# Optimization experiments

Hardware: AMD Instinct MI355X
Metric: run time of the kernel (lower is better)

## Reference

```python
import jax, jax.numpy as jnp
import numpy as np

B, S, H, E, I, MAX_K, A_HID = 2, 2048, 1024, 8, 2688, 6, 50


def setup_inputs() -> dict:
    key = jax.random.key(0)
    ks = jax.random.split(key, 10)
    sc = 0.02
    return {
        "hidden_states": jax.random.normal(ks[0], (B, S, H), dtype=jnp.float32),
        "router_w": jax.random.normal(ks[1], (E, H), dtype=jnp.float32) * sc,
        "actor_w1": jax.random.normal(ks[2], (A_HID, H), dtype=jnp.float32) * sc,
        "actor_b1": jnp.zeros((A_HID,), dtype=jnp.float32),
        "actor_w2": jax.random.normal(ks[3], (MAX_K, A_HID), dtype=jnp.float32) * sc,
        "actor_b2": jnp.zeros((MAX_K,), dtype=jnp.float32),
        "gate_w": jax.random.normal(ks[4], (E, I, H), dtype=jnp.float32) * sc,
        "up_w": jax.random.normal(ks[5], (E, I, H), dtype=jnp.float32) * sc,
        "down_w": jax.random.normal(ks[6], (E, H, I), dtype=jnp.float32) * sc,
    }


def reference(hidden_states, router_w, actor_w1, actor_b1, actor_w2, actor_b2,
              gate_w, up_w, down_w):
    # Router: frozen linear -> softmax probs  [B,S,E]
    probs = jax.nn.softmax(
        jnp.einsum("bsh,eh->bse", hidden_states, router_w).astype(jnp.float32),
        axis=-1)

    # Allocator (ActorCritic.actor): Linear -> GELU -> Linear, clamp(-30,30)
    a_h = jax.nn.gelu(jnp.einsum("bsh,ah->bsa", hidden_states, actor_w1) + actor_b1)
    actor_logits = jnp.clip(
        jnp.einsum("bsa,ka->bsk", a_h, actor_w2) + actor_b2, -30.0, 30.0)
    # deterministic per-token k in [1, MAX_K]
    sampled_k = jnp.argmax(actor_logits, axis=-1) + 1  # [B,S] int

    # dynamic_topk_indices_and_scores: iterative argmax+scatter == select the
    # k highest-prob experts per token; keep their scores, zero elsewhere.
    order = jnp.argsort(-probs, axis=-1)           # descending order of experts
    rank = jnp.argsort(order, axis=-1)             # rank[e] = position of expert e
    mask = rank < sampled_k[..., None]             # [B,S,E] bool, top-k selected
    scores = jnp.where(mask, probs, 0.0).astype(hidden_states.dtype)

    # Expert dispatch-combine: out = sum_e scores[...,e] * LlamaMLP_e(x)
    out = jnp.zeros_like(hidden_states)
    for e in range(E):  # fixed small loop over experts
        g = jnp.einsum("bsh,ih->bsi", hidden_states, gate_w[e])
        u = jnp.einsum("bsh,ih->bsi", hidden_states, up_w[e])
        y = jnp.einsum("bsi,hi->bsh", jax.nn.silu(g) * u, down_w[e])
        out = out + scores[..., e:e + 1] * y
    return out
```

## Files before the change

### kernel.cpp

```cpp
#include <hip/hip_runtime.h>
#include <hip/hip_bf16.h>
#include <stdint.h>

#define TOK 4096
#define HD  1024
#define NE  8
#define ID  2688
#define MAXK 6
#define AHID 50
#define NROW 58
#define KCH 64
#define NCH (HD / KCH)

#define BM 128
#define BN 128
#define BK 64
#define NTM (TOK / BM)
#define NID2 (2 * ID)
#define NTN_GUC (NID2 / BN)
#define NB_GUC (NTN_GUC * NTM)
#define NTN_D (HD / BN)
#define NB_D (NTN_D * NTM)
#define CVTB 384

typedef float  f32x4  __attribute__((ext_vector_type(4)));
typedef __bf16 bf16x8 __attribute__((ext_vector_type(8)));
typedef ushort ushort8v __attribute__((ext_vector_type(8)));

__device__ __forceinline__ ushort f2bf(float f) {
  union { float f; uint32_t u; } v; v.f = f;
  return (ushort)((v.u + 0x7FFFu + ((v.u >> 16) & 1u)) >> 16);
}
__device__ __forceinline__ float bf2f(ushort u) {
  union { uint32_t u; float f; } v; v.u = (uint32_t)u << 16; return v.f;
}

#define GLD_LDS16(gp, lp)                                                      \
  __builtin_amdgcn_global_load_lds(                                            \
      (const __attribute__((address_space(1))) uint32_t*)(uintptr_t)(gp),      \
      (__attribute__((address_space(3))) uint32_t*)(uint32_t)(uintptr_t)(lp),  \
      16, 0, 0)

__global__ void k_cvt(const float* __restrict__ src, ushort* __restrict__ dst, int n) {
  int idx = blockIdx.x * blockDim.x + threadIdx.x;
  int stride = gridDim.x * blockDim.x;
  for (int i = idx * 8; i < n; i += stride * 8) {
    float4 a = *(const float4*)(src + i);
    float4 b = *(const float4*)(src + i + 4);
    ushort8v o;
    o[0] = f2bf(a.x); o[1] = f2bf(a.y); o[2] = f2bf(a.z); o[3] = f2bf(a.w);
    o[4] = f2bf(b.x); o[5] = f2bf(b.y); o[6] = f2bf(b.z); o[7] = f2bf(b.w);
    *(ushort8v*)(dst + i) = o;
  }
}

__global__ void k_cvt_gu(const float* __restrict__ g, const float* __restrict__ u,
                         ushort* __restrict__ dst) {
  const int total = NE * NID2 * (HD / 8);
  int idx = blockIdx.x * blockDim.x + threadIdx.x;
  int stride = gridDim.x * blockDim.x;
  for (int i8 = idx; i8 < total; i8 += stride) {
    const int col = (i8 & (HD / 8 - 1)) * 8;
    const int row = i8 >> 7;
    const int e = row / NID2;
    const int q = row - e * NID2;
    const int p = q >> 7, r = q & 127;
    const float* src = ((r < 64) ? g + ((size_t)e * ID + p * 64 + r) * HD
                                 : u + ((size_t)e * ID + p * 64 + (r - 64)) * HD) + col;
    float4 a = *(const float4*)(src);
    float4 b = *(const float4*)(src + 4);
    ushort8v o;
    o[0] = f2bf(a.x); o[1] = f2bf(a.y); o[2] = f2bf(a.z); o[3] = f2bf(a.w);
    o[4] = f2bf(b.x); o[5] = f2bf(b.y); o[6] = f2bf(b.z); o[7] = f2bf(b.w);
    *(ushort8v*)(dst + (size_t)row * HD + col) = o;
  }
}

__global__ __launch_bounds__(256) void k_logits(
    const float* __restrict__ x, const float* __restrict__ rw,
    const float* __restrict__ aw1, float* __restrict__ partial,
    ushort* __restrict__ Xb) {
  __shared__ float xs[256][KCH + 1];
  const int tid = threadIdx.x;
  const int t0 = blockIdx.x * 256;
  const int c = blockIdx.y;
  const int k0 = c * KCH;
#pragma unroll
  for (int j = 0; j < 16; ++j) {
    const int id4 = j * 256 + tid;
    const int row = id4 >> 4;
    const int c4 = (id4 & 15) * 4;
    float4 v = *(const float4*)(x + (size_t)(t0 + row) * HD + k0 + c4);
    xs[row][c4 + 0] = v.x; xs[row][c4 + 1] = v.y;
    xs[row][c4 + 2] = v.z; xs[row][c4 + 3] = v.w;
    ushort4 o; o.x = f2bf(v.x); o.y = f2bf(v.y); o.z = f2bf(v.z); o.w = f2bf(v.w);
    *(ushort4*)(Xb + (size_t)(t0 + row) * HD + k0 + c4) = o;
  }
  __syncthreads();
  float acc[NROW];
#pragma unroll
  for (int r = 0; r < NROW; ++r) acc[r] = 0.f;
  for (int k4 = 0; k4 < KCH; k4 += 4) {
    const float x0 = xs[tid][k4 + 0], x1 = xs[tid][k4 + 1];
    const float x2 = xs[tid][k4 + 2], x3 = xs[tid][k4 + 3];
#pragma unroll
    for (int r = 0; r < NROW; ++r) {
      const float* wp = ((r < NE) ? (rw + (size_t)r * HD)
                                  : (aw1 + (size_t)(r - NE) * HD)) + k0 + k4;
      acc[r] += x0 * wp[0] + x1 * wp[1] + x2 * wp[2] + x3 * wp[3];
    }
  }
  const int t = t0 + tid;
#pragma unroll
  for (int r = 0; r < NROW; ++r)
    partial[((size_t)c * NROW + r) * TOK + t] = acc[r];
}

__global__ __launch_bounds__(256) void k_reduce(
    const float* __restrict__ partial, float* __restrict__ dots) {
  const int t = blockIdx.x * 256 + threadIdx.x;
  const int r = blockIdx.y;
  float s = 0.f;
#pragma unroll
  for (int c = 0; c < NCH; ++c)
    s += partial[((size_t)c * NROW + r) * TOK + t];
  dots[(size_t)r * TOK + t] = s;
}

__global__ __launch_bounds__(64) void k_select(
    const float* __restrict__ dots, const float* __restrict__ ab1_,
    const float* __restrict__ aw2_, const float* __restrict__ ab2_,
    float* __restrict__ scores, int* __restrict__ idx, int* __restrict__ cnt) {
  const int lane = threadIdx.x;
  const int t = blockIdx.x * 64 + lane;
  float d[NROW];
#pragma unroll
  for (int r = 0; r < NROW; ++r) d[r] = dots[(size_t)r * TOK + t];
  float m = d[0];
#pragma unroll
  for (int e = 1; e < NE; ++e) m = fmaxf(m, d[e]);
  float p[NE]; float sum = 0.f;
#pragma unroll
  for (int e = 0; e < NE; ++e) { p[e] = expf(d[e] - m); sum += p[e]; }
  float inv = 1.f / sum;
#pragma unroll
  for (int e = 0; e < NE; ++e) p[e] *= inv;
  float lg[MAXK];
#pragma unroll
  for (int k = 0; k < MAXK; ++k) lg[k] = ab2_[k];
#pragma unroll
  for (int i = 0; i < AHID; ++i) {
    float v = d[NE + i] + ab1_[i];
    float g = 0.5f * v * (1.f + tanhf(0.7978845608028654f * (v + 0.044715f * v * v * v)));
#pragma unroll
    for (int k = 0; k < MAXK; ++k) lg[k] += g * aw2_[k * AHID + i];
  }
  int best = 0; float bv = fminf(fmaxf(lg[0], -30.f), 30.f);
#pragma unroll
  for (int k = 1; k < MAXK; ++k) {
    float lv = fminf(fmaxf(lg[k], -30.f), 30.f);
    if (lv > bv) { bv = lv; best = k; }
  }
  const int kk = best + 1;
  float sc[NE];
#pragma unroll
  for (int e = 0; e < NE; ++e) {
    int rank = 0;
#pragma unroll
    for (int j = 0; j < NE; ++j)
      rank += (p[j] > p[e]) || (p[j] == p[e] && j < e);
    sc[e] = (rank < kk) ? p[e] : 0.f;
    scores[(size_t)t * NE + e] = sc[e];
  }
#pragma unroll
  for (int e = 0; e < NE; ++e) {
    unsigned long long msk = __ballot(sc[e] > 0.f);
    int npop = __popcll(msk);
    int mypos = __popcll(msk & ((1ull << lane) - 1ull));
    int base = 0;
    if (lane == 0 && npop) base = atomicAdd(cnt + e, npop);
    base = __shfl(base, 0);
    if (sc[e] > 0.f) idx[e * TOK + base + mypos] = t;
  }
}

__global__ __launch_bounds__(256, 2) void k_gateupC(
    const ushort* __restrict__ X, const int* __restrict__ idx,
    const int* __restrict__ cnt, const ushort* __restrict__ Wc,
    ushort* __restrict__ act, const int e0, const int actStrideRows,
    const float* __restrict__ dwsrc, ushort* __restrict__ dwdst) {
  __shared__ __attribute__((aligned(16))) ushort lds[BM * BK + BN * BK];
  ushort* As = lds;
  ushort* Bs = lds + BM * BK;

  const int bid = blockIdx.x;
  if (bid >= NB_GUC) {
    if (blockIdx.z != 0) return;
    const int cb = bid - NB_GUC;
    const int ncvt = NE * HD * ID;
    const int stride = CVTB * 256 * 8;
    for (int i = (cb * 256 + threadIdx.x) * 8; i < ncvt; i += stride) {
      float4 a = *(const float4*)(dwsrc + i);
      float4 b = *(const float4*)(dwsrc + i + 4);
      ushort8v o;
      o[0] = f2bf(a.x); o[1] = f2bf(a.y); o[2] = f2bf(a.z); o[3] = f2bf(a.w);
      o[4] = f2bf(b.x); o[5] = f2bf(b.y); o[6] = f2bf(b.z); o[7] = f2bf(b.w);
      *(ushort8v*)(dwdst + i) = o;
    }
    return;
  }

  const int e = e0 + blockIdx.z;
  const int n = cnt[e];
  const int logical = (bid & 7) * (NB_GUC / 8) + (bid >> 3);
  const int tn = logical >> 5;
  const int tm = logical & (NTM - 1);
  const int row0 = tm * BM;
  if (row0 >= n) return;
  const int* idx_e = idx + e * TOK;
  const ushort* WcE = Wc + (size_t)e * NID2 * HD;
  ushort* actE = act + (size_t)actStrideRows * e * ID;

  const int tid = threadIdx.x;
  const int lane = tid & 63;
  const int w = tid >> 6;
  const int wr = (w >> 1) * 64;
  const int wc = (w & 1) * 64;
  const int srow = lane >> 3;
  const int scol = ((lane & 7) ^ srow) * 8;
  const int col0 = tn * BN;

  f32x4 acc[4][4] = {};

  const ushort* pa[4]; const ushort* pb[4];
  ushort* la[4]; ushort* lb[4];
#pragma unroll
  for (int j = 0; j < 4; ++j) {
    const int cc = w * 4 + j;
    const int r = cc * 8 + srow;
    const int token = idx_e[min(row0 + r, n - 1)];
    pa[j] = X   + (size_t)token * HD + scol;
    pb[j] = WcE + (size_t)(col0 + r) * HD + scol;
    la[j] = &As[cc * 512]; lb[j] = &Bs[cc * 512];
  }

  for (int kt = 0; kt < HD / BK; ++kt) {
    const int k0 = kt * BK;
    __syncthreads();
#pragma unroll
    for (int j = 0; j < 4; ++j) {
      GLD_LDS16(pa[j] + k0, la[j]);
      GLD_LDS16(pb[j] + k0, lb[j]);
    }
    __syncthreads();
#pragma unroll
    for (int kk = 0; kk < 2; ++kk) {
      const int kc = kk * 32 + (lane >> 4) * 8;
      const int rr = lane & 15;
      const int kcs = (((kc >> 3) ^ (rr & 7)) << 3);
      bf16x8 af[4], bf_[4];
#pragma unroll
      for (int m = 0; m < 4; ++m)
        af[m] = *(const bf16x8*)&As[(wr + m * 16 + rr) * BK + kcs];
#pragma unroll
      for (int nn = 0; nn < 4; ++nn)
        bf_[nn] = *(const bf16x8*)&Bs[(wc + nn * 16 + rr) * BK + kcs];
#pragma unroll
      for (int m = 0; m < 4; ++m)
#pragma unroll
        for (int nn = 0; nn < 4; ++nn)
          acc[m][nn] = __builtin_amdgcn_mfma_f32_16x16x32_bf16(af[m], bf_[nn], acc[m][nn], 0, 0, 0);
    }
  }

  const int erow = (lane >> 4) * 4, ecol = lane & 15;
  float* exch = (float*)lds;
  __syncthreads();
  if (w & 1) {
#pragma unroll
    for (int m = 0; m < 4; ++m) {
      const int rbase = wr + m * 16 + erow;
#pragma unroll
      for (int nn = 0; nn < 4; ++nn) {
        const int c = nn * 16 + ecol;
#pragma unroll
        for (int j = 0; j < 4; ++j)
          exch[(rbase + j) * 64 + c] = acc[m][nn][j];
      }
    }
  }
  __syncthreads();
  if (!(w & 1)) {
#pragma unroll
    for (int m = 0; m < 4; ++m) {
      const int rbase = wr + m * 16 + erow;
#pragma unroll
      for (int nn = 0; nn < 4; ++nn) {
        const int c = nn * 16 + ecol;
        const int gc = tn * 64 + c;
#pragma unroll
        for (int j = 0; j < 4; ++j) {
          float g = acc[m][nn][j];
          float u = exch[(rbase + j) * 64 + c];
          float h = (g / (1.f + __expf(-g))) * u;
          actE[(size_t)(row0 + rbase + j) * ID + gc] = f2bf(h);
        }
      }
    }
  }
}

__global__ __launch_bounds__(256, 2) void k_down(
    const ushort* __restrict__ act, const ushort* __restrict__ Wd,
    const int* __restrict__ idx, const int* __restrict__ cnt,
    ushort* __restrict__ y) {
  __shared__ __attribute__((aligned(16))) ushort As[BM * BK];
  __shared__ __attribute__((aligned(16))) ushort Bs[BN * BK];

  const int e = blockIdx.z;
  const int n = cnt[e];
  const int bid = blockIdx.x;
  const int logical = (bid & 7) * (NB_D / 8) + (bid >> 3);
  const int tn = logical >> 5;
  const int tm = logical & (NTM - 1);
  const int row0 = tm * BM;
  if (row0 >= n) return;
  const int* idx_e = idx + e * TOK;
  const ushort* A = act + (size_t)e * TOK * ID;
  const ushort* W = Wd + (size_t)e * HD * ID;
  ushort* yE = y + (size_t)e * TOK * HD;

  const int tid = threadIdx.x;
  const int lane = tid & 63;
  const int w = tid >> 6;
  const int wr = (w >> 1) * 64;
  const int wc = (w & 1) * 64;
  const int srow = lane >> 3;
  const int scol = ((lane & 7) ^ srow) * 8;
  const int col0 = tn * BN;

  f32x4 acc[4][4] = {};

  const ushort* pa[4]; const ushort* pb[4];
  ushort* la[4]; ushort* lb[4];
#pragma unroll
  for (int j = 0; j < 4; ++j) {
    const int cc = w * 4 + j;
    const int r = cc * 8 + srow;
    pa[j] = A + (size_t)min(row0 + r, n - 1) * ID + scol;
    pb[j] = W + (size_t)(col0 + r) * ID + scol;
    la[j] = &As[cc * 512]; lb[j] = &Bs[cc * 512];
  }

  for (int kt = 0; kt < ID / BK; ++kt) {
    const int k0 = kt * BK;
    __syncthreads();
#pragma unroll
    for (int j = 0; j < 4; ++j) {
      GLD_LDS16(pa[j] + k0, la[j]);
      GLD_LDS16(pb[j] + k0, lb[j]);
    }
    __syncthreads();
#pragma unroll
    for (int kk = 0; kk < 2; ++kk) {
      const int kc = kk * 32 + (lane >> 4) * 8;
      const int rr = lane & 15;
      const int kcs = (((kc >> 3) ^ (rr & 7)) << 3);
      bf16x8 af[4], bf_[4];
#pragma unroll
      for (int m = 0; m < 4; ++m)
        af[m] = *(const bf16x8*)&As[(wr + m * 16 + rr) * BK + kcs];
#pragma unroll
      for (int nn = 0; nn < 4; ++nn)
        bf_[nn] = *(const bf16x8*)&Bs[(wc + nn * 16 + rr) * BK + kcs];
#pragma unroll
      for (int m = 0; m < 4; ++m)
#pragma unroll
        for (int nn = 0; nn < 4; ++nn)
          acc[m][nn] = __builtin_amdgcn_mfma_f32_16x16x32_bf16(af[m], bf_[nn], acc[m][nn], 0, 0, 0);
    }
  }

  const int erow = (lane >> 4) * 4, ecol = lane & 15;
#pragma unroll
  for (int m = 0; m < 4; ++m) {
    const int cr0 = row0 + wr + m * 16 + erow;
#pragma unroll
    for (int j = 0; j < 4; ++j) {
      const int cr = cr0 + j;
      if (cr < n) {
        const int token = idx_e[cr];
        ushort* yp = yE + (size_t)token * HD + col0 + wc;
#pragma unroll
        for (int nn = 0; nn < 4; ++nn)
          yp[nn * 16 + ecol] = f2bf(acc[m][nn][j]);
      }
    }
  }
}

__global__ __launch_bounds__(256) void k_combine(
    const ushort* __restrict__ y, const float* __restrict__ scores,
    float* __restrict__ out) {
  const int w = threadIdx.x >> 6, lane = threadIdx.x & 63;
  const int t = blockIdx.x * 4 + w;
  const int c0 = lane * 16;
  float acc[16];
#pragma unroll
  for (int i = 0; i < 16; ++i) acc[i] = 0.f;
  const float* sc = scores + (size_t)t * NE;
#pragma unroll
  for (int e = 0; e < NE; ++e) {
    const float s = sc[e];
    if (s > 0.f) {
      const ushort8v* yp = (const ushort8v*)(y + ((size_t)e * TOK + t) * HD + c0);
      ushort8v v0 = yp[0], v1 = yp[1];
#pragma unroll
      for (int i = 0; i < 8; ++i) acc[i] += s * bf2f(v0[i]);
#pragma unroll
      for (int i = 0; i < 8; ++i) acc[8 + i] += s * bf2f(v1[i]);
    }
  }
  float* op = out + (size_t)t * HD + c0;
#pragma unroll
  for (int i = 0; i < 4; ++i)
    *(float4*)(op + 4 * i) = make_float4(acc[4*i], acc[4*i+1], acc[4*i+2], acc[4*i+3]);
}

__global__ __launch_bounds__(256) void k_down64(
    const ushort* __restrict__ act, const ushort* __restrict__ Wd,
    const float* __restrict__ scores, const int* __restrict__ idx,
    const int* __restrict__ cnt, const int e, float* __restrict__ out) {
  __shared__ __attribute__((aligned(16))) ushort As[64 * 64];
  __shared__ __attribute__((aligned(16))) ushort Bs[64 * 64];
  const int n = cnt[e];
  const int row0 = blockIdx.y * 64;
  if (row0 >= n) return;
  const int* idx_e = idx + e * TOK;
  const ushort* A = act;
  const ushort* W = Wd + (size_t)e * HD * ID;
  const int col0 = blockIdx.x * 64;
  const int tid = threadIdx.x, lane = tid & 63, w = tid >> 6;
  const int wr = (w >> 1) * 32, wc = (w & 1) * 32;
  const int srow = lane >> 3, scol = (lane & 7) * 8;
  f32x4 acc[2][2] = {};
  const ushort* pa[2]; const ushort* pb[2];
  ushort* la[2]; ushort* lb[2];
#pragma unroll
  for (int j = 0; j < 2; ++j) {
    const int cc = w * 2 + j;
    const int r = cc * 8 + srow;
    pa[j] = A + (size_t)min(row0 + r, n - 1) * ID + scol;
    pb[j] = W + (size_t)(col0 + r) * ID + scol;
    la[j] = &As[cc * 512]; lb[j] = &Bs[cc * 512];
  }
  for (int kt = 0; kt < ID / 64; ++kt) {
    const int k0 = kt * 64;
    __syncthreads();
#pragma unroll
    for (int j = 0; j < 2; ++j) { GLD_LDS16(pa[j] + k0, la[j]); GLD_LDS16(pb[j] + k0, lb[j]); }
    __syncthreads();
#pragma unroll
    for (int kk = 0; kk < 2; ++kk) {
      const int kc = kk * 32 + (lane >> 4) * 8;
      const int rr = lane & 15;
      bf16x8 af[2], bf_[2];
#pragma unroll
      for (int m = 0; m < 2; ++m) af[m] = *(const bf16x8*)&As[(wr + m * 16 + rr) * 64 + kc];
#pragma unroll
      for (int nn = 0; nn < 2; ++nn) bf_[nn] = *(const bf16x8*)&Bs[(wc + nn * 16 + rr) * 64 + kc];
#pragma unroll
      for (int m = 0; m < 2; ++m)
#pragma unroll
        for (int nn = 0; nn < 2; ++nn)
          acc[m][nn] = __builtin_amdgcn_mfma_f32_16x16x32_bf16(af[m], bf_[nn], acc[m][nn], 0, 0, 0);
    }
  }
  const int erow = (lane >> 4) * 4, ecol = lane & 15;
#pragma unroll
  for (int m = 0; m < 2; ++m) {
    const int cr0 = row0 + wr + m * 16 + erow;
#pragma unroll
    for (int j = 0; j < 4; ++j) {
      const int cr = cr0 + j;
      if (cr < n) {
        const int token = idx_e[cr];
        const float s = scores[(size_t)token * NE + e];
        float* op = out + (size_t)token * HD + col0 + wc;
#pragma unroll
        for (int nn = 0; nn < 2; ++nn) op[nn * 16 + ecol] += s * acc[m][nn][j];
      }
    }
  }
}

extern "C" void kernel_launch(void* const* d_in, const int* in_sizes, int n_in,
                              void* d_out, int out_size, void* d_ws, size_t ws_size,
                              hipStream_t stream) {
  const float* hs       = (const float*)d_in[0];
  const float* router_w = (const float*)d_in[1];
  const float* actor_w1 = (const float*)d_in[2];
  const float* actor_b1 = (const float*)d_in[3];
  const float* actor_w2 = (const float*)d_in[4];
  const float* actor_b2 = (const float*)d_in[5];
  const float* gate_w   = (const float*)d_in[6];
  const float* up_w     = (const float*)d_in[7];
  const float* down_w   = (const float*)d_in[8];
  float* out = (float*)d_out;

  const size_t sz_x    = (size_t)TOK * HD * 2;
  const size_t sz_w    = (size_t)NE * ID * HD * 2;
  const size_t sz_wgu  = 2 * sz_w;
  const size_t sz_act1 = (size_t)TOK * ID * 2;
  const size_t sz_actC = (size_t)NE * TOK * ID * 2;
  const size_t sz_part = (size_t)NCH * NROW * TOK * 4;
  const size_t sz_dt   = (size_t)NROW * TOK * 4;
  const size_t sz_sc   = (size_t)TOK * NE * 4;
  const size_t sz_ix   = (size_t)NE * TOK * 4;

  const size_t fixed = sz_x + sz_wgu + sz_w;
  const size_t tail  = sz_dt + sz_sc + sz_ix + 256;
  const size_t fb_act = (sz_act1 > sz_part ? sz_act1 : sz_part);
  const size_t need_fb = fixed + fb_act + tail;
  const size_t need_cb = fixed + sz_actC + tail;
  if (ws_size < need_fb) return;
  const bool combined = (ws_size >= need_cb);
  const size_t act_sz = combined ? sz_actC : fb_act;

  char* ws = (char*)d_ws;
  ushort* Xb  = (ushort*)ws;
  ushort* Wgu = (ushort*)(ws + sz_x);
  ushort* Wdb = (ushort*)(ws + sz_x + sz_wgu);
  ushort* yb  = Wgu;
  ushort* act = (ushort*)(ws + fixed);
  float*  partial = (float*)(ws + fixed);
  float*  dots   = (float*)(ws + fixed + act_sz);
  float*  scores = (float*)(ws + fixed + act_sz + sz_dt);
  int*    idx    = (int*)  (ws + fixed + act_sz + sz_dt + sz_sc);
  int*    cnt    = (int*)  (ws + fixed + act_sz + sz_dt + sz_sc + sz_ix);

  hipMemsetAsync(cnt, 0, NE * 4, stream);

  k_cvt_gu<<<2048, 256, 0, stream>>>(gate_w, up_w, Wgu);

  k_logits<<<dim3(TOK / 256, NCH), 256, 0, stream>>>(hs, router_w, actor_w1, partial, Xb);
  k_reduce<<<dim3(TOK / 256, NROW), 256, 0, stream>>>(partial, dots);
  k_select<<<TOK / 64, 64, 0, stream>>>(dots, actor_b1, actor_w2, actor_b2,
                                        scores, idx, cnt);

  if (combined) {
    k_gateupC<<<dim3(NB_GUC + CVTB, 1, NE), 256, 0, stream>>>(
        Xb, idx, cnt, Wgu, act, 0, TOK, down_w, Wdb);
    k_down<<<dim3(NB_D, 1, NE), 256, 0, stream>>>(act, Wdb, idx, cnt, yb);
    k_combine<<<TOK / 4, 256, 0, stream>>>(yb, scores, out);
  } else {
    hipMemsetAsync(out, 0, (size_t)TOK * HD * 4, stream);
    k_cvt<<<2048, 256, 0, stream>>>(down_w, Wdb, NE * ID * HD);
    for (int e = 0; e < NE; ++e) {
      k_gateupC<<<dim3(NB_GUC, 1, 1), 256, 0, stream>>>(
          Xb, idx, cnt, Wgu, act, e, 0, nullptr, nullptr);
      k_down64<<<dim3(HD / 64, TOK / 64), 256, 0, stream>>>(
          act, Wdb, scores, idx, cnt, e, out);
    }
  }
}
```

Before: 480.9 us.

## Replace expert GEMMs with 256x256-tile, 8-wave, double-buffered pipelined kernels

The gate/up and down expert GEMMs move from 128x128 tiles with 4 waves and a load-sync-compute loop to 256x256 tiles with 8 waves. They use a double-buffered LDS stage split into k-halves, so async global-to-LDS loads for the next step overlap MFMA work, with explicit vmcnt waits, barriers and s_setprio around the MFMA bursts. The larger tile raises data reuse per block and cuts the number of blocks. The tradeoff is 128KB of LDS per block, fewer blocks for small expert token counts, and a more complex hand-scheduled pipeline that could raise register pressure.

```diff
diff --git a/kernel.cpp b/kernel.cpp
--- a/kernel.cpp
+++ b/kernel.cpp
@@ -19,9 +19,10 @@
 #define NID2 (2 * ID)
 #define NTN_GUC (NID2 / BN)
 #define NB_GUC (NTN_GUC * NTM)
-#define NTN_D (HD / BN)
-#define NB_D (NTN_D * NTM)
-#define CVTB 384
+#define CVTB8 160
+
+#define NB8_GU (21 * 16)
+#define NB8_D  (4 * 16)
 
 typedef float  f32x4  __attribute__((ext_vector_type(4)));
 typedef __bf16 bf16x8 __attribute__((ext_vector_type(8)));
@@ -184,22 +185,47 @@
   }
 }
 
-__global__ __launch_bounds__(256, 2) void k_gateupC(
+
+#define STG8(PTR0, PTR1, LBASE, koff)                                          \
+  do {                                                                         \
+    GLD_LDS16((PTR0) + (koff), (LBASE));                                       \
+    GLD_LDS16((PTR1) + (koff), (LBASE) + 512);                                 \
+  } while (0)
+
+#define PH8(kh_, q_, RDB_)                                                     \
+  {                                                                            \
+    const int reg_ = (buf * 2 + (kh_)) * 8192;                                 \
+    bf16x8 af_[4];                                                             \
+    _Pragma("unroll") for (int mm = 0; mm < 4; ++mm)                           \
+        af_[mm] = *(const bf16x8*)&SH[reg_ + baseA + ((q_)*64 + mm*16) * 32];  \
+    if (RDB_) {                                                                \
+      _Pragma("unroll") for (int nn = 0; nn < 4; ++nn)                         \
+          bfr[nn] = *(const bf16x8*)&SH[32768 + reg_ + baseB + nn * 16 * 32];  \
+    }                                                                          \
+    __builtin_amdgcn_s_barrier();                                              \
+    __builtin_amdgcn_s_setprio(1);                                             \
+    _Pragma("unroll") for (int mm = 0; mm < 4; ++mm)                           \
+    _Pragma("unroll") for (int nn = 0; nn < 4; ++nn)                           \
+        acc[(q_)*4 + mm][nn] = __builtin_amdgcn_mfma_f32_16x16x32_bf16(        \
+            af_[mm], bfr[nn], acc[(q_)*4 + mm][nn], 0, 0, 0);                  \
+    __builtin_amdgcn_s_setprio(0);                                             \
+    __builtin_amdgcn_s_barrier();                                              \
+  }
+
+__global__ __launch_bounds__(512, 2) void k_gateup8(
     const ushort* __restrict__ X, const int* __restrict__ idx,
     const int* __restrict__ cnt, const ushort* __restrict__ Wc,
-    ushort* __restrict__ act, const int e0, const int actStrideRows,
+    ushort* __restrict__ act,
     const float* __restrict__ dwsrc, ushort* __restrict__ dwdst) {
-  __shared__ __attribute__((aligned(16))) ushort lds[BM * BK + BN * BK];
-  ushort* As = lds;
-  ushort* Bs = lds + BM * BK;
+  __shared__ __attribute__((aligned(16))) ushort SH[65536];
 
   const int bid = blockIdx.x;
-  if (bid >= NB_GUC) {
+  if (bid >= NB8_GU) {
     if (blockIdx.z != 0) return;
-    const int cb = bid - NB_GUC;
+    const int cb = bid - NB8_GU;
     const int ncvt = NE * HD * ID;
-    const int stride = CVTB * 256 * 8;
-    for (int i = (cb * 256 + threadIdx.x) * 8; i < ncvt; i += stride) {
+    const int stride = CVTB8 * 512 * 8;
+    for (int i = (cb * 512 + (int)threadIdx.x) * 8; i < ncvt; i += stride) {
       float4 a = *(const float4*)(dwsrc + i);
       float4 b = *(const float4*)(dwsrc + i + 4);
       ushort8v o;
@@ -210,8 +236,235 @@
     return;
   }
 
-  const int e = e0 + blockIdx.z;
+  const int e = blockIdx.z;
   const int n = cnt[e];
+  const int logical = (bid & 7) * (NB8_GU / 8) + (bid >> 3);
+  const int tn = logical >> 4;
+  const int tm = logical & 15;
+  const int row0 = tm * 256;
+  if (row0 >= n) return;
+  const int* idx_e = idx + e * TOK;
+  const ushort* WcE = Wc + (size_t)e * NID2 * HD;
+  ushort* actE = act + (size_t)e * TOK * ID;
+  const int col0 = tn * 256;
+
+  const int tid = threadIdx.x;
+  const int lane = tid & 63;
+  const int w = tid >> 6;
+  const int wm = w >> 2;
+  const int wn = w & 3;
+
+  const int lr = lane >> 2;
+  const int swzS = (((lane & 3) ^ (lr & 3)) << 3);
+  const int rA0 = w * 32 + lr, rA1 = w * 32 + 16 + lr;
+  const ushort* pA0 = X + (size_t)idx_e[min(row0 + rA0, n - 1)] * HD + swzS;
+  const ushort* pA1 = X + (size_t)idx_e[min(row0 + rA1, n - 1)] * HD + swzS;
+  const ushort* pB0 = WcE + (size_t)(col0 + rA0) * HD + swzS;
+  const ushort* pB1 = WcE + (size_t)(col0 + rA1) * HD + swzS;
+  const int lgrp = (w * 32) * 32;
+
+  const int rl = lane & 15, gk = lane >> 4;
+  const int rsw = ((gk ^ (rl & 3)) << 3);
+  const int baseA = (wm * 128 + rl) * 32 + rsw;
+  const int baseB = (wn * 64 + rl) * 32 + rsw;
+
+  f32x4 acc[8][4] = {};
+  bf16x8 bfr[4];
+
+  const int NT = HD / BK;
+#define SA8(t_, kh_) STG8(pA0, pA1, SH + ((((t_)&1)*2 + (kh_)) * 8192) + lgrp, (t_)*BK + (kh_)*32)
+#define SB8(t_, kh_) STG8(pB0, pB1, SH + 32768 + ((((t_)&1)*2 + (kh_)) * 8192) + lgrp, (t_)*BK + (kh_)*32)
+
+  SA8(0, 0); SB8(0, 0); SA8(0, 1); SB8(0, 1);
+  SA8(1, 0); SB8(1, 0);
+  asm volatile("s_waitcnt vmcnt(4)" ::: "memory");
+  __builtin_amdgcn_s_barrier();
+
+  for (int t = 0; t < NT; ++t) {
+    const int buf = t & 1;
+    if (t + 1 < NT) SA8(t + 1, 1);
+    PH8(0, 0, 1)
+    if (t + 1 < NT) SB8(t + 1, 1);
+    PH8(0, 1, 0)
+    if (t + 2 < NT) SA8(t + 2, 0);
+    PH8(1, 0, 1)
+    if (t + 2 < NT) SB8(t + 2, 0);
+    if (t + 1 < NT) {
+      if (t + 2 < NT) { asm volatile("s_waitcnt vmcnt(4)" ::: "memory"); }
+      else            { asm volatile("s_waitcnt vmcnt(0)" ::: "memory"); }
+    }
+    PH8(1, 1, 0)
+  }
+#undef SA8
+#undef SB8
+
+  const int erow = (lane >> 4) * 4, ecol = lane & 15;
+  const int slot = wm * 2 + (wn >> 1);
+  float* exch = (float*)SH;
+  if (wn & 1) {
+#pragma unroll
+    for (int mm = 0; mm < 8; ++mm) {
+      const int rb = mm * 16 + erow;
+#pragma unroll
+      for (int nn = 0; nn < 4; ++nn) {
+        const int cc = nn * 16 + ecol;
+#pragma unroll
+        for (int j = 0; j < 4; ++j)
+          exch[(slot * 128 + rb + j) * 64 + cc] = acc[mm][nn][j];
+      }
+    }
+  }
+  __builtin_amdgcn_s_barrier();
+  if (!(wn & 1)) {
+    const int p = tn * 2 + (wn >> 1);
+#pragma unroll
+    for (int mm = 0; mm < 8; ++mm) {
+      const int rb = mm * 16 + erow;
+#pragma unroll
+      for (int nn = 0; nn < 4; ++nn) {
+        const int cc = nn * 16 + ecol;
+        const int gc = p * 64 + cc;
+#pragma unroll
+        for (int j = 0; j < 4; ++j) {
+          const int cr = row0 + wm * 128 + rb + j;
+          if (cr < n) {
+            float g = acc[mm][nn][j];
+            float u = exch[(slot * 128 + rb + j) * 64 + cc];
+            float h = (g / (1.f + __expf(-g))) * u;
+            actE[(size_t)cr * ID + gc] = f2bf(h);
+          }
+        }
+      }
+    }
+  }
+}
+
+__global__ __launch_bounds__(512, 2) void k_down8(
+    const ushort* __restrict__ act, const ushort* __restrict__ Wd,
+    const int* __restrict__ idx, const int* __restrict__ cnt,
+    ushort* __restrict__ y) {
+  __shared__ __attribute__((aligned(16))) ushort SH[65536];
+
+  const int e = blockIdx.z;
+  const int n = cnt[e];
+  const int bid = blockIdx.x;
+  const int logical = (bid & 7) * (NB8_D / 8) + (bid >> 3);
+  const int tn = logical >> 4;
+  const int tm = logical & 15;
+  const int row0 = tm * 256;
+  if (row0 >= n) return;
+  const int* idx_e = idx + e * TOK;
+  const ushort* A = act + (size_t)e * TOK * ID;
+  const ushort* W = Wd + (size_t)e * HD * ID;
+  ushort* yE = y + (size_t)e * TOK * HD;
+  const int col0 = tn * 256;
+
+  const int tid = threadIdx.x;
+  const int lane = tid & 63;
+  const int w = tid >> 6;
+  const int wm = w >> 2;
+  const int wn = w & 3;
+
+  const int lr = lane >> 2;
+  const int swzS = (((lane & 3) ^ (lr & 3)) << 3);
+  const int rA0 = w * 32 + lr, rA1 = w * 32 + 16 + lr;
+  const ushort* pA0 = A + (size_t)min(row0 + rA0, n - 1) * ID + swzS;
+  const ushort* pA1 = A + (size_t)min(row0 + rA1, n - 1) * ID + swzS;
+  const ushort* pB0 = W + (size_t)(col0 + rA0) * ID + swzS;
+  const ushort* pB1 = W + (size_t)(col0 + rA1) * ID + swzS;
+  const int lgrp = (w * 32) * 32;
+
+  const int rl = lane & 15, gk = lane >> 4;
+  const int rsw = ((gk ^ (rl & 3)) << 3);
+  const int baseA = (wm * 128 + rl) * 32 + rsw;
+  const int baseB = (wn * 64 + rl) * 32 + rsw;
+
+  f32x4 acc[8][4] = {};
+  bf16x8 bfr[4];
+
+  const int NT = ID / BK;
+#define SA8(t_, kh_) STG8(pA0, pA1, SH + ((((t_)&1)*2 + (kh_)) * 8192) + lgrp, (t_)*BK + (kh_)*32)
+#define SB8(t_, kh_) STG8(pB0, pB1, SH + 32768 + ((((t_)&1)*2 + (kh_)) * 8192) + lgrp, (t_)*BK + (kh_)*32)
+
+  SA8(0, 0); SB8(0, 0); SA8(0, 1); SB8(0, 1);
+  SA8(1, 0); SB8(1, 0);
+  asm volatile("s_waitcnt vmcnt(4)" ::: "memory");
+  __builtin_amdgcn_s_barrier();
+
+  for (int t = 0; t < NT; ++t) {
+    const int buf = t & 1;
+    if (t + 1 < NT) SA8(t + 1, 1);
+    PH8(0, 0, 1)
+    if (t + 1 < NT) SB8(t + 1, 1);
+    PH8(0, 1, 0)
+    if (t + 2 < NT) SA8(t + 2, 0);
+    PH8(1, 0, 1)
+    if (t + 2 < NT) SB8(t + 2, 0);
+    if (t + 1 < NT) {
+      if (t + 2 < NT) { asm volatile("s_waitcnt vmcnt(4)" ::: "memory"); }
+      else            { asm volatile("s_waitcnt vmcnt(0)" ::: "memory"); }
+    }
+    PH8(1, 1, 0)
+  }
+#undef SA8
+#undef SB8
+
+  const int erow = (lane >> 4) * 4, ecol = lane & 15;
+#pragma unroll
+  for (int mm = 0; mm < 8; ++mm) {
+    const int cr0 = row0 + wm * 128 + mm * 16 + erow;
+#pragma unroll
+    for (int j = 0; j < 4; ++j) {
+      const int cr = cr0 + j;
+      if (cr < n) {
+        const int token = idx_e[cr];
+        ushort* yp = yE + (size_t)token * HD + col0 + wn * 64;
+#pragma unroll
+        for (int nn = 0; nn < 4; ++nn)
+          yp[nn * 16 + ecol] = f2bf(acc[mm][nn][j]);
+      }
+    }
+  }
+}
+
+__global__ __launch_bounds__(256) void k_combine(
+    const ushort* __restrict__ y, const float* __restrict__ scores,
+    float* __restrict__ out) {
+  const int w = threadIdx.x >> 6, lane = threadIdx.x & 63;
+  const int t = blockIdx.x * 4 + w;
+  const int c0 = lane * 16;
+  float acc[16];
+#pragma unroll
+  for (int i = 0; i < 16; ++i) acc[i] = 0.f;
+  const float* sc = scores + (size_t)t * NE;
+#pragma unroll
+  for (int e = 0; e < NE; ++e) {
+    const float s = sc[e];
+    if (s > 0.f) {
+      const ushort8v* yp = (const ushort8v*)(y + ((size_t)e * TOK + t) * HD + c0);
+      ushort8v v0 = yp[0], v1 = yp[1];
+#pragma unroll
+      for (int i = 0; i < 8; ++i) acc[i] += s * bf2f(v0[i]);
+#pragma unroll
+      for (int i = 0; i < 8; ++i) acc[8 + i] += s * bf2f(v1[i]);
+    }
+  }
+  float* op = out + (size_t)t * HD + c0;
+#pragma unroll
+  for (int i = 0; i < 4; ++i)
+    *(float4*)(op + 4 * i) = make_float4(acc[4*i], acc[4*i+1], acc[4*i+2], acc[4*i+3]);
+}
+
+__global__ __launch_bounds__(256, 2) void k_gateupC(
+    const ushort* __restrict__ X, const int* __restrict__ idx,
+    const int* __restrict__ cnt, const ushort* __restrict__ Wc,
+    ushort* __restrict__ act, const int e0) {
+  __shared__ __attribute__((aligned(16))) ushort lds[BM * BK + BN * BK];
+  ushort* As = lds;
+  ushort* Bs = lds + BM * BK;
+  const int e = e0;
+  const int n = cnt[e];
+  const int bid = blockIdx.x;
   const int logical = (bid & 7) * (NB_GUC / 8) + (bid >> 3);
   const int tn = logical >> 5;
   const int tm = logical & (NTM - 1);
@@ -219,19 +472,13 @@
   if (row0 >= n) return;
   const int* idx_e = idx + e * TOK;
   const ushort* WcE = Wc + (size_t)e * NID2 * HD;
-  ushort* actE = act + (size_t)actStrideRows * e * ID;
-
-  const int tid = threadIdx.x;
-  const int lane = tid & 63;
-  const int w = tid >> 6;
-  const int wr = (w >> 1) * 64;
-  const int wc = (w & 1) * 64;
+  ushort* actE = act;
+  const int tid = threadIdx.x, lane = tid & 63, w = tid >> 6;
+  const int wr = (w >> 1) * 64, wc = (w & 1) * 64;
   const int srow = lane >> 3;
   const int scol = ((lane & 7) ^ srow) * 8;
   const int col0 = tn * BN;
-
   f32x4 acc[4][4] = {};
-
   const ushort* pa[4]; const ushort* pb[4];
   ushort* la[4]; ushort* lb[4];
 #pragma unroll
@@ -239,19 +486,15 @@
     const int cc = w * 4 + j;
     const int r = cc * 8 + srow;
     const int token = idx_e[min(row0 + r, n - 1)];
-    pa[j] = X   + (size_t)token * HD + scol;
+    pa[j] = X + (size_t)token * HD + scol;
     pb[j] = WcE + (size_t)(col0 + r) * HD + scol;
     la[j] = &As[cc * 512]; lb[j] = &Bs[cc * 512];
   }
-
   for (int kt = 0; kt < HD / BK; ++kt) {
     const int k0 = kt * BK;
     __syncthreads();
 #pragma unroll
-    for (int j = 0; j < 4; ++j) {
-      GLD_LDS16(pa[j] + k0, la[j]);
-      GLD_LDS16(pb[j] + k0, lb[j]);
-    }
+    for (int j = 0; j < 4; ++j) { GLD_LDS16(pa[j] + k0, la[j]); GLD_LDS16(pb[j] + k0, lb[j]); }
     __syncthreads();
 #pragma unroll
     for (int kk = 0; kk < 2; ++kk) {
@@ -260,11 +503,9 @@
       const int kcs = (((kc >> 3) ^ (rr & 7)) << 3);
       bf16x8 af[4], bf_[4];
 #pragma unroll
-      for (int m = 0; m < 4; ++m)
-        af[m] = *(const bf16x8*)&As[(wr + m * 16 + rr) * BK + kcs];
-#pragma unroll
-      for (int nn = 0; nn < 4; ++nn)
-        bf_[nn] = *(const bf16x8*)&Bs[(wc + nn * 16 + rr) * BK + kcs];
+      for (int m = 0; m < 4; ++m) af[m] = *(const bf16x8*)&As[(wr + m * 16 + rr) * BK + kcs];
+#pragma unroll
+      for (int nn = 0; nn < 4; ++nn) bf_[nn] = *(const bf16x8*)&Bs[(wc + nn * 16 + rr) * BK + kcs];
 #pragma unroll
       for (int m = 0; m < 4; ++m)
 #pragma unroll
@@ -272,7 +513,6 @@
           acc[m][nn] = __builtin_amdgcn_mfma_f32_16x16x32_bf16(af[m], bf_[nn], acc[m][nn], 0, 0, 0);
     }
   }
-
   const int erow = (lane >> 4) * 4, ecol = lane & 15;
   float* exch = (float*)lds;
   __syncthreads();
@@ -284,8 +524,7 @@
       for (int nn = 0; nn < 4; ++nn) {
         const int c = nn * 16 + ecol;
 #pragma unroll
-        for (int j = 0; j < 4; ++j)
-          exch[(rbase + j) * 64 + c] = acc[m][nn][j];
+        for (int j = 0; j < 4; ++j) exch[(rbase + j) * 64 + c] = acc[m][nn][j];
       }
     }
   }
@@ -308,123 +547,6 @@
       }
     }
   }
-}
-
-__global__ __launch_bounds__(256, 2) void k_down(
-    const ushort* __restrict__ act, const ushort* __restrict__ Wd,
-    const int* __restrict__ idx, const int* __restrict__ cnt,
-    ushort* __restrict__ y) {
-  __shared__ __attribute__((aligned(16))) ushort As[BM * BK];
-  __shared__ __attribute__((aligned(16))) ushort Bs[BN * BK];
-
-  const int e = blockIdx.z;
-  const int n = cnt[e];
-  const int bid = blockIdx.x;
-  const int logical = (bid & 7) * (NB_D / 8) + (bid >> 3);
-  const int tn = logical >> 5;
-  const int tm = logical & (NTM - 1);
-  const int row0 = tm * BM;
-  if (row0 >= n) return;
-  const int* idx_e = idx + e * TOK;
-  const ushort* A = act + (size_t)e * TOK * ID;
-  const ushort* W = Wd + (size_t)e * HD * ID;
-  ushort* yE = y + (size_t)e * TOK * HD;
-
-  const int tid = threadIdx.x;
-  const int lane = tid & 63;
-  const int w = tid >> 6;
-  const int wr = (w >> 1) * 64;
-  const int wc = (w & 1) * 64;
-  const int srow = lane >> 3;
-  const int scol = ((lane & 7) ^ srow) * 8;
-  const int col0 = tn * BN;
-
-  f32x4 acc[4][4] = {};
-
-  const ushort* pa[4]; const ushort* pb[4];
-  ushort* la[4]; ushort* lb[4];
-#pragma unroll
-  for (int j = 0; j < 4; ++j) {
-    const int cc = w * 4 + j;
-    const int r = cc * 8 + srow;
-    pa[j] = A + (size_t)min(row0 + r, n - 1) * ID + scol;
-    pb[j] = W + (size_t)(col0 + r) * ID + scol;
-    la[j] = &As[cc * 512]; lb[j] = &Bs[cc * 512];
-  }
-
-  for (int kt = 0; kt < ID / BK; ++kt) {
-    const int k0 = kt * BK;
-    __syncthreads();
-#pragma unroll
-    for (int j = 0; j < 4; ++j) {
-      GLD_LDS16(pa[j] + k0, la[j]);
-      GLD_LDS16(pb[j] + k0, lb[j]);
-    }
-    __syncthreads();
-#pragma unroll
-    for (int kk = 0; kk < 2; ++kk) {
-      const int kc = kk * 32 + (lane >> 4) * 8;
-      const int rr = lane & 15;
-      const int kcs = (((kc >> 3) ^ (rr & 7)) << 3);
-      bf16x8 af[4], bf_[4];
-#pragma unroll
-      for (int m = 0; m < 4; ++m)
-        af[m] = *(const bf16x8*)&As[(wr + m * 16 + rr) * BK + kcs];
-#pragma unroll
-      for (int nn = 0; nn < 4; ++nn)
-        bf_[nn] = *(const bf16x8*)&Bs[(wc + nn * 16 + rr) * BK + kcs];
-#pragma unroll
-      for (int m = 0; m < 4; ++m)
-#pragma unroll
-        for (int nn = 0; nn < 4; ++nn)
-          acc[m][nn] = __builtin_amdgcn_mfma_f32_16x16x32_bf16(af[m], bf_[nn], acc[m][nn], 0, 0, 0);
-    }
-  }
-
-  const int erow = (lane >> 4) * 4, ecol = lane & 15;
-#pragma unroll
-  for (int m = 0; m < 4; ++m) {
-    const int cr0 = row0 + wr + m * 16 + erow;
-#pragma unroll
-    for (int j = 0; j < 4; ++j) {
-      const int cr = cr0 + j;
-      if (cr < n) {
-        const int token = idx_e[cr];
-        ushort* yp = yE + (size_t)token * HD + col0 + wc;
-#pragma unroll
-        for (int nn = 0; nn < 4; ++nn)
-          yp[nn * 16 + ecol] = f2bf(acc[m][nn][j]);
-      }
-    }
-  }
-}
-
-__global__ __launch_bounds__(256) void k_combine(
-    const ushort* __restrict__ y, const float* __restrict__ scores,
-    float* __restrict__ out) {
-  const int w = threadIdx.x >> 6, lane = threadIdx.x & 63;
-  const int t = blockIdx.x * 4 + w;
-  const int c0 = lane * 16;
-  float acc[16];
-#pragma unroll
-  for (int i = 0; i < 16; ++i) acc[i] = 0.f;
-  const float* sc = scores + (size_t)t * NE;
-#pragma unroll
-  for (int e = 0; e < NE; ++e) {
-    const float s = sc[e];
-    if (s > 0.f) {
-      const ushort8v* yp = (const ushort8v*)(y + ((size_t)e * TOK + t) * HD + c0);
-      ushort8v v0 = yp[0], v1 = yp[1];
-#pragma unroll
-      for (int i = 0; i < 8; ++i) acc[i] += s * bf2f(v0[i]);
-#pragma unroll
-      for (int i = 0; i < 8; ++i) acc[8 + i] += s * bf2f(v1[i]);
-    }
-  }
-  float* op = out + (size_t)t * HD + c0;
-#pragma unroll
-  for (int i = 0; i < 4; ++i)
-    *(float4*)(op + 4 * i) = make_float4(acc[4*i], acc[4*i+1], acc[4*i+2], acc[4*i+3]);
 }
 
 __global__ __launch_bounds__(256) void k_down64(
@@ -549,16 +671,15 @@
                                         scores, idx, cnt);
 
   if (combined) {
-    k_gateupC<<<dim3(NB_GUC + CVTB, 1, NE), 256, 0, stream>>>(
-        Xb, idx, cnt, Wgu, act, 0, TOK, down_w, Wdb);
-    k_down<<<dim3(NB_D, 1, NE), 256, 0, stream>>>(act, Wdb, idx, cnt, yb);
+    k_gateup8<<<dim3(NB8_GU + CVTB8, 1, NE), 512, 0, stream>>>(
+        Xb, idx, cnt, Wgu, act, down_w, Wdb);
+    k_down8<<<dim3(NB8_D, 1, NE), 512, 0, stream>>>(act, Wdb, idx, cnt, yb);
     k_combine<<<TOK / 4, 256, 0, stream>>>(yb, scores, out);
   } else {
     hipMemsetAsync(out, 0, (size_t)TOK * HD * 4, stream);
     k_cvt<<<2048, 256, 0, stream>>>(down_w, Wdb, NE * ID * HD);
     for (int e = 0; e < NE; ++e) {
-      k_gateupC<<<dim3(NB_GUC, 1, 1), 256, 0, stream>>>(
-          Xb, idx, cnt, Wgu, act, e, 0, nullptr, nullptr);
+      k_gateupC<<<dim3(NB_GUC, 1, 1), 256, 0, stream>>>(Xb, idx, cnt, Wgu, act, e);
       k_down64<<<dim3(HD / 64, TOK / 64), 256, 0, stream>>>(
           act, Wdb, scores, idx, cnt, e, out);
     }
```

New measurement: 618.9 us. 1.29x slower.

## Rewrite down-projection GEMM as 256x256 tile, 8-wave, 4-stage pipelined kernel

Applied to the files above, without the earlier changes.

Replaces the 128x128 single-buffered down-projection GEMM with a 256x256 tile kernel using 512 threads and 128KB of LDS. Inputs stream through a 4-deep ring buffer with direct global-to-LDS loads, explicit vmcnt waits and split A/B prefetch interleaved with MFMA phases, plus s_setprio around the math. This is meant to hide load latency and raise arithmetic intensity per byte loaded. In exchange it has far fewer blocks per expert, so load balance suffers when per-expert token counts are small.

```diff
diff --git a/kernel.cpp b/kernel.cpp
--- a/kernel.cpp
+++ b/kernel.cpp
@@ -19,9 +19,8 @@
 #define NID2 (2 * ID)
 #define NTN_GUC (NID2 / BN)
 #define NB_GUC (NTN_GUC * NTM)
-#define NTN_D (HD / BN)
-#define NB_D (NTN_D * NTM)
 #define CVTB 384
+#define NB4_D 64
 
 typedef float  f32x4  __attribute__((ext_vector_type(4)));
 typedef __bf16 bf16x8 __attribute__((ext_vector_type(8)));
@@ -199,7 +198,7 @@
     const int cb = bid - NB_GUC;
     const int ncvt = NE * HD * ID;
     const int stride = CVTB * 256 * 8;
-    for (int i = (cb * 256 + threadIdx.x) * 8; i < ncvt; i += stride) {
+    for (int i = (cb * 256 + (int)threadIdx.x) * 8; i < ncvt; i += stride) {
       float4 a = *(const float4*)(dwsrc + i);
       float4 b = *(const float4*)(dwsrc + i + 4);
       ushort8v o;
@@ -310,90 +309,108 @@
   }
 }
 
-__global__ __launch_bounds__(256, 2) void k_down(
+__global__ __launch_bounds__(512, 2) void k_down4r(
     const ushort* __restrict__ act, const ushort* __restrict__ Wd,
     const int* __restrict__ idx, const int* __restrict__ cnt,
     ushort* __restrict__ y) {
-  __shared__ __attribute__((aligned(16))) ushort As[BM * BK];
-  __shared__ __attribute__((aligned(16))) ushort Bs[BN * BK];
+  __shared__ __attribute__((aligned(16))) ushort SH[65536];
 
   const int e = blockIdx.z;
   const int n = cnt[e];
   const int bid = blockIdx.x;
-  const int logical = (bid & 7) * (NB_D / 8) + (bid >> 3);
-  const int tn = logical >> 5;
-  const int tm = logical & (NTM - 1);
-  const int row0 = tm * BM;
+  const int logical = (bid & 7) * (NB4_D / 8) + (bid >> 3);
+  const int tn = logical >> 4;
+  const int tm = logical & 15;
+  const int row0 = tm * 256;
   if (row0 >= n) return;
   const int* idx_e = idx + e * TOK;
   const ushort* A = act + (size_t)e * TOK * ID;
   const ushort* W = Wd + (size_t)e * HD * ID;
   ushort* yE = y + (size_t)e * TOK * HD;
-
-  const int tid = threadIdx.x;
-  const int lane = tid & 63;
-  const int w = tid >> 6;
-  const int wr = (w >> 1) * 64;
-  const int wc = (w & 1) * 64;
-  const int srow = lane >> 3;
-  const int scol = ((lane & 7) ^ srow) * 8;
-  const int col0 = tn * BN;
-
-  f32x4 acc[4][4] = {};
-
-  const ushort* pa[4]; const ushort* pb[4];
-  ushort* la[4]; ushort* lb[4];
-#pragma unroll
-  for (int j = 0; j < 4; ++j) {
-    const int cc = w * 4 + j;
-    const int r = cc * 8 + srow;
-    pa[j] = A + (size_t)min(row0 + r, n - 1) * ID + scol;
-    pb[j] = W + (size_t)(col0 + r) * ID + scol;
-    la[j] = &As[cc * 512]; lb[j] = &Bs[cc * 512];
-  }
-
-  for (int kt = 0; kt < ID / BK; ++kt) {
-    const int k0 = kt * BK;
-    __syncthreads();
-#pragma unroll
-    for (int j = 0; j < 4; ++j) {
-      GLD_LDS16(pa[j] + k0, la[j]);
-      GLD_LDS16(pb[j] + k0, lb[j]);
-    }
-    __syncthreads();
-#pragma unroll
-    for (int kk = 0; kk < 2; ++kk) {
-      const int kc = kk * 32 + (lane >> 4) * 8;
-      const int rr = lane & 15;
-      const int kcs = (((kc >> 3) ^ (rr & 7)) << 3);
-      bf16x8 af[4], bf_[4];
-#pragma unroll
-      for (int m = 0; m < 4; ++m)
-        af[m] = *(const bf16x8*)&As[(wr + m * 16 + rr) * BK + kcs];
+  const int col0 = tn * 256;
+
+  const int tid = threadIdx.x, lane = tid & 63, w = tid >> 6;
+  const int wm = w >> 2, wn = w & 3;
+  const int rl = lane & 15, gk = lane >> 4;
+
+  const int srcswz = ((lane & 3) ^ ((lane >> 2) & 3) ^ ((lane >> 4) & 3)) * 8;
+  const int r0s = w * 32 + (lane >> 2);
+  const ushort* pA0 = A + (size_t)min(row0 + r0s,      n - 1) * ID + srcswz;
+  const ushort* pA1 = A + (size_t)min(row0 + r0s + 16, n - 1) * ID + srcswz;
+  const ushort* pB0 = W + (size_t)(col0 + r0s)      * ID + srcswz;
+  const ushort* pB1 = W + (size_t)(col0 + r0s + 16) * ID + srcswz;
+  const int ldsW = w * 1024;
+
+  const int swzrd = (gk ^ (rl & 3) ^ ((rl >> 2) & 3)) * 8;
+  const int aBase = wm * 4096 + rl * 32 + swzrd;
+  const int bBase = 32768 + wn * 2048 + rl * 32 + swzrd;
+
+  f32x4 acc[8][4] = {};
+
+#define SA4(t_) do { GLD_LDS16(pA0 + (t_)*32, SH + ((t_)&3)*8192 + ldsW);        \
+                     GLD_LDS16(pA1 + (t_)*32, SH + ((t_)&3)*8192 + ldsW + 512); } while (0)
+#define SB4(t_) do { GLD_LDS16(pB0 + (t_)*32, SH + 32768 + ((t_)&3)*8192 + ldsW);        \
+                     GLD_LDS16(pB1 + (t_)*32, SH + 32768 + ((t_)&3)*8192 + ldsW + 512); } while (0)
+
+  SA4(0); SB4(0); SA4(1); SB4(1); SA4(2); SB4(2);
+  asm volatile("s_waitcnt vmcnt(8)" ::: "memory");
+  __builtin_amdgcn_s_barrier();
+
+  const int NT = ID / 32;
+  for (int T = 0; T < NT; ++T) {
+    const int buf = (T & 3) * 8192;
+    bf16x8 af[4], bf_[4];
+    if (T + 3 < NT) SA4(T + 3);
+#pragma unroll
+    for (int mm = 0; mm < 4; ++mm)
+      af[mm] = *(const bf16x8*)&SH[buf + aBase + mm * 512];
+#pragma unroll
+    for (int nn = 0; nn < 4; ++nn)
+      bf_[nn] = *(const bf16x8*)&SH[buf + bBase + nn * 512];
+    __builtin_amdgcn_s_barrier();
+    __builtin_amdgcn_s_setprio(1);
+#pragma unroll
+    for (int mm = 0; mm < 4; ++mm)
 #pragma unroll
       for (int nn = 0; nn < 4; ++nn)
-        bf_[nn] = *(const bf16x8*)&Bs[(wc + nn * 16 + rr) * BK + kcs];
-#pragma unroll
-      for (int m = 0; m < 4; ++m)
-#pragma unroll
-        for (int nn = 0; nn < 4; ++nn)
-          acc[m][nn] = __builtin_amdgcn_mfma_f32_16x16x32_bf16(af[m], bf_[nn], acc[m][nn], 0, 0, 0);
-    }
-  }
-
-  const int erow = (lane >> 4) * 4, ecol = lane & 15;
-#pragma unroll
-  for (int m = 0; m < 4; ++m) {
-    const int cr0 = row0 + wr + m * 16 + erow;
+        acc[mm][nn] = __builtin_amdgcn_mfma_f32_16x16x32_bf16(af[mm], bf_[nn], acc[mm][nn], 0, 0, 0);
+    __builtin_amdgcn_s_setprio(0);
+    __builtin_amdgcn_s_barrier();
+    if (T + 3 < NT) SB4(T + 3);
+#pragma unroll
+    for (int mm = 0; mm < 4; ++mm)
+      af[mm] = *(const bf16x8*)&SH[buf + aBase + (4 + mm) * 512];
+    if (T + 1 < NT) {
+      if (T + 3 < NT)      { asm volatile("s_waitcnt vmcnt(8)" ::: "memory"); }
+      else if (T + 2 < NT) { asm volatile("s_waitcnt vmcnt(4)" ::: "memory"); }
+      else                 { asm volatile("s_waitcnt vmcnt(0)" ::: "memory"); }
+    }
+    __builtin_amdgcn_s_barrier();
+    __builtin_amdgcn_s_setprio(1);
+#pragma unroll
+    for (int mm = 0; mm < 4; ++mm)
+#pragma unroll
+      for (int nn = 0; nn < 4; ++nn)
+        acc[4 + mm][nn] = __builtin_amdgcn_mfma_f32_16x16x32_bf16(af[mm], bf_[nn], acc[4 + mm][nn], 0, 0, 0);
+    __builtin_amdgcn_s_setprio(0);
+    __builtin_amdgcn_s_barrier();
+  }
+#undef SA4
+#undef SB4
+
+  const int erow = gk * 4, ecol = rl;
+#pragma unroll
+  for (int mm = 0; mm < 8; ++mm) {
+    const int cr0 = row0 + wm * 128 + mm * 16 + erow;
 #pragma unroll
     for (int j = 0; j < 4; ++j) {
       const int cr = cr0 + j;
       if (cr < n) {
         const int token = idx_e[cr];
-        ushort* yp = yE + (size_t)token * HD + col0 + wc;
+        ushort* yp = yE + (size_t)token * HD + col0 + wn * 64;
 #pragma unroll
         for (int nn = 0; nn < 4; ++nn)
-          yp[nn * 16 + ecol] = f2bf(acc[m][nn][j]);
+          yp[nn * 16 + ecol] = f2bf(acc[mm][nn][j]);
       }
     }
   }
@@ -551,7 +568,7 @@
   if (combined) {
     k_gateupC<<<dim3(NB_GUC + CVTB, 1, NE), 256, 0, stream>>>(
         Xb, idx, cnt, Wgu, act, 0, TOK, down_w, Wdb);
-    k_down<<<dim3(NB_D, 1, NE), 256, 0, stream>>>(act, Wdb, idx, cnt, yb);
+    k_down4r<<<dim3(NB4_D, 1, NE), 512, 0, stream>>>(act, Wdb, idx, cnt, yb);
     k_combine<<<TOK / 4, 256, 0, stream>>>(yb, scores, out);
   } else {
     hipMemsetAsync(out, 0, (size_t)TOK * HD * 4, stream);
```

New measurement: 535.7 us. 11.4% more time.
